# Kernel optimization log

Measured on AMD Instinct MI355X. Metric: run time of the kernel, lower is better.

## Reference

```python
import jax, jax.numpy as jnp
import numpy as np

TAU = 2.0          # LIF membrane time constant (spikingjelly default)
V_TH = 1.0         # v_threshold
V_RESET = 0.0      # hard reset value
ATAN_ALPHA = 2.0   # surrogate.ATan default alpha
EPS = 1e-12        # F.normalize eps

@jax.custom_vjp
def spike_fn(x):
    # Heaviside forward, ATan surrogate backward
    return (x >= 0).astype(x.dtype)

def _spike_fwd(x):
    return spike_fn(x), x

def _spike_bwd(x, g):
    sg = (ATAN_ALPHA / 2.0) / (1.0 + (jnp.pi / 2.0 * ATAN_ALPHA * x) ** 2)
    return (g * sg,)

spike_fn.defvjp(_spike_fwd, _spike_bwd)

def setup_inputs() -> dict:
    key = jax.random.key(0)
    k1, k2 = jax.random.split(key)
    T, B, F, H = 32, 512, 2048, 2048
    x_seq = jax.random.normal(k1, (T, B, F), dtype=jnp.float32)
    lim = float(np.sqrt(6.0 / (F + H)))  # xavier_uniform
    W = jax.random.uniform(k2, (H, F), dtype=jnp.float32, minval=-lim, maxval=lim)
    b = jnp.zeros((H,), dtype=jnp.float32)
    return {"x_seq": x_seq, "W": W, "b": b}

def reference(x_seq, W, b):
    # Linear: [T,B,F] @ [F,H] -> [T,B,H]
    cur = jnp.einsum('tbf,hf->tbh', x_seq, W) + b
    # F.normalize(dim=-1): L2 normalize the injected current per neuron vector
    norm = jnp.maximum(jnp.sqrt(jnp.sum(cur * cur, axis=-1, keepdims=True)), EPS)
    cur = cur / norm

    def step(v, c):
        # LIF charge: v <- v + (x - (v - v_reset)) / tau
        v = v + (c - (v - V_RESET)) / TAU
        s = spike_fn(v - V_TH)
        sd = jax.lax.stop_gradient(s)  # detach_reset=True
        v = v * (1.0 - sd) + V_RESET * sd  # hard reset
        return v, s

    v0 = jnp.zeros(cur.shape[1:], dtype=cur.dtype)  # [B,H]
    _, spk_seq = jax.lax.scan(step, v0, cur)  # spk_seq: [T,B,H]
    count = spk_seq.sum(axis=0)  # [B,H]
    return spk_seq, count
```

## Files before the change

kernel.cpp:

```cpp
#include <hip/hip_runtime.h>
#include <hip/hip_bf16.h>

#define T_SZ 32
#define B_SZ 512
#define F_SZ 2048
#define H_SZ 2048
#define M_SZ (T_SZ * B_SZ)

#define BM 128
#define BN 128
#define BK 128

typedef int   i32x8  __attribute__((ext_vector_type(8)));
typedef float f32x16 __attribute__((ext_vector_type(16)));
typedef unsigned short u16x8 __attribute__((ext_vector_type(8)));

__device__ __forceinline__ void gload_lds16(const void* g, void* l) {
    __builtin_amdgcn_global_load_lds(
        (const __attribute__((address_space(1))) unsigned int*)g,
        (__attribute__((address_space(3))) unsigned int*)l,
        16, 0, 0);
}

__device__ __forceinline__ float bf16_bits_to_f32(unsigned short u) {
    return __uint_as_float(((unsigned)u) << 16);
}

__global__ __launch_bounds__(256) void cvt_fp8_kernel(const float* __restrict__ in,
                                                      unsigned int* __restrict__ out,
                                                      float scale, int n8) {
    int i = blockIdx.x * 256 + threadIdx.x;
    if (i >= n8) return;
    float4 v0 = ((const float4*)in)[2 * i];
    float4 v1 = ((const float4*)in)[2 * i + 1];
    int w0 = __builtin_amdgcn_cvt_pk_fp8_f32(v0.x * scale, v0.y * scale, 0, false);
    w0     = __builtin_amdgcn_cvt_pk_fp8_f32(v0.z * scale, v0.w * scale, w0, true);
    int w1 = __builtin_amdgcn_cvt_pk_fp8_f32(v1.x * scale, v1.y * scale, 0, false);
    w1     = __builtin_amdgcn_cvt_pk_fp8_f32(v1.z * scale, v1.w * scale, w1, true);
    ((uint2*)out)[i] = make_uint2((unsigned)w0, (unsigned)w1);
}

__global__ __launch_bounds__(256) void init_ss_kernel(float4* __restrict__ ss4) {
    ss4[blockIdx.x * 256 + threadIdx.x] = make_float4(0.f, 0.f, 0.f, 0.f);
}

__global__ __launch_bounds__(256, 3) void gemm_fp8_kernel(const unsigned char* __restrict__ A,
                                                          const unsigned char* __restrict__ Bt,
                                                          const float* __restrict__ bias,
                                                          __hip_bfloat16* __restrict__ C,
                                                          float* __restrict__ ss)
{
    __shared__ __align__(16) unsigned char As[BM * BK];
    __shared__ __align__(16) unsigned char Bs[BN * BK];

    const int tid  = threadIdx.x;
    const int lane = tid & 63;
    const int wave = tid >> 6;
    const int wm   = wave >> 1;
    const int wn   = wave & 1;
    const int m0   = blockIdx.y * BM;
    const int n0   = blockIdx.x * BN;
    const int l31  = lane & 31;
    const int kh   = lane >> 5;

    f32x16 acc[2][2] = {};

    for (int k0 = 0; k0 < F_SZ; k0 += BK) {
        __syncthreads();
        #pragma unroll
        for (int j = 0; j < 4; ++j) {
            int c   = j * 256 + tid;
            int row = c >> 3;
            int u   = (c & 7) ^ (row & 7);
            gload_lds16(A + (size_t)(m0 + row) * F_SZ + k0 + u * 16, (void*)(As + c * 16));
        }
        #pragma unroll
        for (int j = 0; j < 4; ++j) {
            int c   = j * 256 + tid;
            int row = c >> 3;
            int u   = (c & 7) ^ (row & 7);
            gload_lds16(Bt + (size_t)(n0 + row) * F_SZ + k0 + u * 16, (void*)(Bs + c * 16));
        }
        __syncthreads();

        #pragma unroll
        for (int s = 0; s < 2; ++s) {
            i32x8 af[2], bq[2];
            #pragma unroll
            for (int i = 0; i < 2; ++i) {
                const int ra = wm * 64 + i * 32 + l31;
                const int rb = wn * 64 + i * 32 + l31;
                const int ua = s * 4 + kh * 2;
                ((int4*)&af[i])[0] = *(const int4*)(As + ra * BK + (((ua + 0) ^ (ra & 7)) * 16));
                ((int4*)&af[i])[1] = *(const int4*)(As + ra * BK + (((ua + 1) ^ (ra & 7)) * 16));
                ((int4*)&bq[i])[0] = *(const int4*)(Bs + rb * BK + (((ua + 0) ^ (rb & 7)) * 16));
                ((int4*)&bq[i])[1] = *(const int4*)(Bs + rb * BK + (((ua + 1) ^ (rb & 7)) * 16));
            }
            #pragma unroll
            for (int mi = 0; mi < 2; ++mi)
                #pragma unroll
                for (int ni = 0; ni < 2; ++ni)
                    acc[mi][ni] = __builtin_amdgcn_mfma_scale_f32_32x32x64_f8f6f4(
                        af[mi], bq[ni], acc[mi][ni],
                        0 , 0 ,
                        0, 0x7f7f7f7f,
                        0, 0x7f7f7f7f);
        }
    }

    float ssl[2][16];
    #pragma unroll
    for (int ni = 0; ni < 2; ++ni) {
        const int gn = n0 + wn * 64 + ni * 32 + l31;
        const float bv = bias[gn];
        #pragma unroll
        for (int mi = 0; mi < 2; ++mi) {
            const int gmb = m0 + wm * 64 + mi * 32 + 4 * kh;
            #pragma unroll
            for (int r = 0; r < 16; ++r) {
                const int grow = gmb + (r & 3) + 8 * (r >> 2);
                const float val = acc[mi][ni][r] * (1.0f / 256.0f) + bv;
                C[(size_t)grow * H_SZ + gn] = __float2bfloat16(val);
                if (ni == 0) ssl[mi][r] = val * val;
                else         ssl[mi][r] += val * val;
            }
        }
    }
    #pragma unroll
    for (int mi = 0; mi < 2; ++mi) {
        const int gmb = m0 + wm * 64 + mi * 32 + 4 * kh;
        #pragma unroll
        for (int r = 0; r < 16; ++r) {
            float p = ssl[mi][r];
            p += __shfl_xor(p, 1, 64);
            p += __shfl_xor(p, 2, 64);
            p += __shfl_xor(p, 4, 64);
            p += __shfl_xor(p, 8, 64);
            p += __shfl_xor(p, 16, 64);
            if (l31 == 0)
                atomicAdd(ss + gmb + (r & 3) + 8 * (r >> 2), p);
        }
    }
}

__global__ __launch_bounds__(256) void lif_scan_kernel(const __hip_bfloat16* __restrict__ cur,
                                                       const float* __restrict__ ss,
                                                       float* __restrict__ spk,
                                                       float* __restrict__ cnt)
{
    const int gid = blockIdx.x * 256 + threadIdx.x;
    const int b   = gid >> 9;
    const int h0  = (gid & 511) * 4;

    float v[4]  = {0, 0, 0, 0};
    float cn[4] = {0, 0, 0, 0};
    #pragma unroll
    for (int t = 0; t < T_SZ; ++t) {
        const size_t off = (size_t)(t * B_SZ + b) * H_SZ + h0;
        const ushort4 pk = *(const ushort4*)(cur + off);
        const float inv  = 1.0f / fmaxf(sqrtf(ss[t * B_SZ + b]), 1e-12f);
        float so[4];
        {
            float c;
            c = bf16_bits_to_f32(pk.x) * inv; v[0] += (c - v[0]) * 0.5f;
            c = bf16_bits_to_f32(pk.y) * inv; v[1] += (c - v[1]) * 0.5f;
            c = bf16_bits_to_f32(pk.z) * inv; v[2] += (c - v[2]) * 0.5f;
            c = bf16_bits_to_f32(pk.w) * inv; v[3] += (c - v[3]) * 0.5f;
        }
        #pragma unroll
        for (int j = 0; j < 4; ++j) {
            float s = (v[j] >= 1.0f) ? 1.0f : 0.0f;
            so[j] = s;
            cn[j] += s;
            v[j] = (s != 0.f) ? 0.f : v[j];
        }
        *(float4*)(spk + off) = make_float4(so[0], so[1], so[2], so[3]);
    }
    *(float4*)(cnt + (size_t)b * H_SZ + h0) = make_float4(cn[0], cn[1], cn[2], cn[3]);
}

extern "C" void kernel_launch(void* const* d_in, const int* in_sizes, int n_in,
                              void* d_out, int out_size, void* d_ws, size_t ws_size,
                              hipStream_t stream) {
    const float* x    = (const float*)d_in[0];
    const float* W    = (const float*)d_in[1];
    const float* bias = (const float*)d_in[2];

    float* spk = (float*)d_out;
    float* cnt = spk + (size_t)T_SZ * B_SZ * H_SZ;

    char* ws = (char*)d_ws;
    unsigned char* x8    = (unsigned char*)ws;
    unsigned char* W8    = x8 + (size_t)M_SZ * F_SZ;
    __hip_bfloat16* curb = (__hip_bfloat16*)(W8 + (size_t)H_SZ * F_SZ);
    float* ss            = (float*)((char*)curb + (size_t)M_SZ * H_SZ * 2);

    init_ss_kernel<<<M_SZ / 1024, 256, 0, stream>>>((float4*)ss);
    cvt_fp8_kernel<<<(M_SZ * F_SZ / 8) / 256, 256, 0, stream>>>(x, (unsigned int*)x8, 1.0f,   M_SZ * F_SZ / 8);
    cvt_fp8_kernel<<<(H_SZ * F_SZ / 8) / 256, 256, 0, stream>>>(W, (unsigned int*)W8, 256.0f, H_SZ * F_SZ / 8);
    gemm_fp8_kernel<<<dim3(H_SZ / BN, M_SZ / BM), 256, 0, stream>>>(x8, W8, bias, curb, ss);
    lif_scan_kernel<<<(B_SZ * H_SZ / 4) / 256, 256, 0, stream>>>(curb, ss, spk, cnt);
}
```

Before: 357.2 us.

## Enlarge FP8 GEMM tiles to 256x256 with double-buffered LDS pipeline and prefetch LIF inputs

Doubles the GEMM block tile to 256x256 with 8 waves. It stages global-to-LDS loads into a ping-pong buffer that is issued in quarter chunks interleaved with the MFMA work, and adds raised wave priority and explicit barriers. Block indices are remapped so that neighbouring blocks share A and B panels in L2. The LIF scan now precomputes per-timestep inverse norms in shared memory and software-prefetches three timesteps of bf16 current. The costs are larger LDS use (128KB per block), more register pressure, and hand-tuned vmcnt waits that could be fragile.

```diff
diff --git a/kernel.cpp b/kernel.cpp
--- a/kernel.cpp
+++ b/kernel.cpp
@@ -7,13 +7,15 @@
 #define H_SZ 2048
 #define M_SZ (T_SZ * B_SZ)
 
-#define BM 128
-#define BN 128
+#define BM 256
+#define BN 256
 #define BK 128
+#define NT (F_SZ / BK)
+#define BUF_BYTES  65536
+#define HALF_BYTES 16384
 
 typedef int   i32x8  __attribute__((ext_vector_type(8)));
 typedef float f32x16 __attribute__((ext_vector_type(16)));
-typedef unsigned short u16x8 __attribute__((ext_vector_type(8)));
 
 __device__ __forceinline__ void gload_lds16(const void* g, void* l) {
     __builtin_amdgcn_global_load_lds(
@@ -24,6 +26,24 @@
 
 __device__ __forceinline__ float bf16_bits_to_f32(unsigned short u) {
     return __uint_as_float(((unsigned)u) << 16);
+}
+
+__device__ __forceinline__ void sbar() {
+    __builtin_amdgcn_sched_barrier(0);
+    __builtin_amdgcn_s_barrier();
+    __builtin_amdgcn_sched_barrier(0);
+}
+
+__device__ __forceinline__ void stage_half_tile(unsigned char* lds,
+                                                const unsigned char* gpanel,
+                                                int kbyte, int tid) {
+    #pragma unroll
+    for (int j = 0; j < 2; ++j) {
+        int c   = j * 512 + tid;
+        int row = c >> 3;
+        int u   = (c & 7) ^ (row & 7);
+        gload_lds16(gpanel + (size_t)row * F_SZ + kbyte + u * 16, (void*)(lds + c * 16));
+    }
 }
 
 __global__ __launch_bounds__(256) void cvt_fp8_kernel(const float* __restrict__ in,
@@ -44,101 +64,125 @@
     ss4[blockIdx.x * 256 + threadIdx.x] = make_float4(0.f, 0.f, 0.f, 0.f);
 }
 
-__global__ __launch_bounds__(256, 3) void gemm_fp8_kernel(const unsigned char* __restrict__ A,
+__global__ __launch_bounds__(512, 2) void gemm_fp8_kernel(const unsigned char* __restrict__ A,
                                                           const unsigned char* __restrict__ Bt,
                                                           const float* __restrict__ bias,
                                                           __hip_bfloat16* __restrict__ C,
                                                           float* __restrict__ ss)
 {
-    __shared__ __align__(16) unsigned char As[BM * BK];
-    __shared__ __align__(16) unsigned char Bs[BN * BK];
+    __shared__ __align__(16) unsigned char smem[2 * BUF_BYTES];
 
     const int tid  = threadIdx.x;
     const int lane = tid & 63;
     const int wave = tid >> 6;
-    const int wm   = wave >> 1;
-    const int wn   = wave & 1;
-    const int m0   = blockIdx.y * BM;
-    const int n0   = blockIdx.x * BN;
+    const int wm   = wave >> 2;
+    const int wn   = wave & 3;
     const int l31  = lane & 31;
     const int kh   = lane >> 5;
 
-    f32x16 acc[2][2] = {};
-
-    for (int k0 = 0; k0 < F_SZ; k0 += BK) {
-        __syncthreads();
-        #pragma unroll
-        for (int j = 0; j < 4; ++j) {
-            int c   = j * 256 + tid;
-            int row = c >> 3;
-            int u   = (c & 7) ^ (row & 7);
-            gload_lds16(A + (size_t)(m0 + row) * F_SZ + k0 + u * 16, (void*)(As + c * 16));
-        }
-        #pragma unroll
-        for (int j = 0; j < 4; ++j) {
-            int c   = j * 256 + tid;
-            int row = c >> 3;
-            int u   = (c & 7) ^ (row & 7);
-            gload_lds16(Bt + (size_t)(n0 + row) * F_SZ + k0 + u * 16, (void*)(Bs + c * 16));
-        }
-        __syncthreads();
-
-        #pragma unroll
-        for (int s = 0; s < 2; ++s) {
-            i32x8 af[2], bq[2];
-            #pragma unroll
-            for (int i = 0; i < 2; ++i) {
-                const int ra = wm * 64 + i * 32 + l31;
-                const int rb = wn * 64 + i * 32 + l31;
+    const int flat = blockIdx.y * 8 + blockIdx.x;
+    const int swz  = (flat & 7) * 64 + (flat >> 3);
+    const int n0   = (swz & 7) * BN;
+    const int m0   = (swz >> 3) * BM;
+
+    f32x16 acc[4][2] = {};
+
+    stage_half_tile(smem + 32768,              Bt + (size_t)(n0      ) * F_SZ, 0, tid);
+    stage_half_tile(smem + 32768 + HALF_BYTES, Bt + (size_t)(n0 + 128) * F_SZ, 0, tid);
+    stage_half_tile(smem,                      A  + (size_t)(m0      ) * F_SZ, 0, tid);
+    stage_half_tile(smem + HALF_BYTES,         A  + (size_t)(m0 + 128) * F_SZ, 0, tid);
+    stage_half_tile(smem + BUF_BYTES + 32768,              Bt + (size_t)(n0      ) * F_SZ, BK, tid);
+    stage_half_tile(smem + BUF_BYTES + 32768 + HALF_BYTES, Bt + (size_t)(n0 + 128) * F_SZ, BK, tid);
+    asm volatile("s_waitcnt vmcnt(4)" ::: "memory");
+    sbar();
+
+    #pragma unroll 1
+    for (int kt = 0; kt < NT; ++kt) {
+        const int cur = kt & 1;
+        const int nxt = cur ^ 1;
+        unsigned char* const As = smem + cur * BUF_BYTES;
+        unsigned char* const Bs = As + 32768;
+
+        auto read_af = [&](i32x8* dst, int mi) {
+            const int ra = wm * 128 + mi * 32 + l31;
+            #pragma unroll
+            for (int s = 0; s < 2; ++s) {
                 const int ua = s * 4 + kh * 2;
-                ((int4*)&af[i])[0] = *(const int4*)(As + ra * BK + (((ua + 0) ^ (ra & 7)) * 16));
-                ((int4*)&af[i])[1] = *(const int4*)(As + ra * BK + (((ua + 1) ^ (ra & 7)) * 16));
-                ((int4*)&bq[i])[0] = *(const int4*)(Bs + rb * BK + (((ua + 0) ^ (rb & 7)) * 16));
-                ((int4*)&bq[i])[1] = *(const int4*)(Bs + rb * BK + (((ua + 1) ^ (rb & 7)) * 16));
+                ((int4*)&dst[s])[0] = *(const int4*)(As + ra * BK + (((ua + 0) ^ (ra & 7)) * 16));
+                ((int4*)&dst[s])[1] = *(const int4*)(As + ra * BK + (((ua + 1) ^ (ra & 7)) * 16));
             }
-            #pragma unroll
-            for (int mi = 0; mi < 2; ++mi)
+        };
+
+        i32x8 bq[2][2];
+        #pragma unroll
+        for (int ni = 0; ni < 2; ++ni) {
+            const int rb = wn * 64 + ni * 32 + l31;
+            #pragma unroll
+            for (int s = 0; s < 2; ++s) {
+                const int ua = s * 4 + kh * 2;
+                ((int4*)&bq[ni][s])[0] = *(const int4*)(Bs + rb * BK + (((ua + 0) ^ (rb & 7)) * 16));
+                ((int4*)&bq[ni][s])[1] = *(const int4*)(Bs + rb * BK + (((ua + 1) ^ (rb & 7)) * 16));
+            }
+        }
+        i32x8 af[2][2];
+        read_af(af[0], 0);
+
+        #pragma unroll
+        for (int mi = 0; mi < 4; ++mi) {
+            if (mi < 3) read_af(af[(mi + 1) & 1], mi + 1);
+
+            if (mi == 0 && kt < NT - 1)
+                stage_half_tile(smem + nxt * BUF_BYTES,              A  + (size_t)(m0      ) * F_SZ, (kt + 1) * BK, tid);
+            if (mi == 1 && kt < NT - 1)
+                stage_half_tile(smem + nxt * BUF_BYTES + HALF_BYTES, A  + (size_t)(m0 + 128) * F_SZ, (kt + 1) * BK, tid);
+            if (mi == 2 && kt < NT - 2)
+                stage_half_tile(smem + cur * BUF_BYTES + 32768,              Bt + (size_t)(n0      ) * F_SZ, (kt + 2) * BK, tid);
+            if (mi == 3 && kt < NT - 2)
+                stage_half_tile(smem + cur * BUF_BYTES + 32768 + HALF_BYTES, Bt + (size_t)(n0 + 128) * F_SZ, (kt + 2) * BK, tid);
+
+            __builtin_amdgcn_sched_barrier(0);
+            __builtin_amdgcn_s_setprio(1);
+            #pragma unroll
+            for (int ni = 0; ni < 2; ++ni)
                 #pragma unroll
-                for (int ni = 0; ni < 2; ++ni)
+                for (int s = 0; s < 2; ++s)
                     acc[mi][ni] = __builtin_amdgcn_mfma_scale_f32_32x32x64_f8f6f4(
-                        af[mi], bq[ni], acc[mi][ni],
+                        af[mi & 1][s], bq[ni][s], acc[mi][ni],
                         0 , 0 ,
                         0, 0x7f7f7f7f,
                         0, 0x7f7f7f7f);
-        }
-    }
-
-    float ssl[2][16];
-    #pragma unroll
-    for (int ni = 0; ni < 2; ++ni) {
-        const int gn = n0 + wn * 64 + ni * 32 + l31;
-        const float bv = bias[gn];
-        #pragma unroll
-        for (int mi = 0; mi < 2; ++mi) {
-            const int gmb = m0 + wm * 64 + mi * 32 + 4 * kh;
-            #pragma unroll
-            for (int r = 0; r < 16; ++r) {
-                const int grow = gmb + (r & 3) + 8 * (r >> 2);
-                const float val = acc[mi][ni][r] * (1.0f / 256.0f) + bv;
+            __builtin_amdgcn_s_setprio(0);
+            if (mi < 3) sbar();
+        }
+
+        if (kt <= NT - 3)      { asm volatile("s_waitcnt vmcnt(4)" ::: "memory"); }
+        else if (kt == NT - 2) { asm volatile("s_waitcnt vmcnt(0)" ::: "memory"); }
+        sbar();
+    }
+
+    float bv[2];
+    #pragma unroll
+    for (int ni = 0; ni < 2; ++ni) bv[ni] = bias[n0 + wn * 64 + ni * 32 + l31];
+    #pragma unroll
+    for (int mi = 0; mi < 4; ++mi) {
+        const int gmb = m0 + wm * 128 + mi * 32 + 4 * kh;
+        #pragma unroll
+        for (int r = 0; r < 16; ++r) {
+            const int grow = gmb + (r & 3) + 8 * (r >> 2);
+            float p = 0.f;
+            #pragma unroll
+            for (int ni = 0; ni < 2; ++ni) {
+                const int gn = n0 + wn * 64 + ni * 32 + l31;
+                const float val = acc[mi][ni][r] * (1.0f / 256.0f) + bv[ni];
                 C[(size_t)grow * H_SZ + gn] = __float2bfloat16(val);
-                if (ni == 0) ssl[mi][r] = val * val;
-                else         ssl[mi][r] += val * val;
+                p += val * val;
             }
-        }
-    }
-    #pragma unroll
-    for (int mi = 0; mi < 2; ++mi) {
-        const int gmb = m0 + wm * 64 + mi * 32 + 4 * kh;
-        #pragma unroll
-        for (int r = 0; r < 16; ++r) {
-            float p = ssl[mi][r];
             p += __shfl_xor(p, 1, 64);
             p += __shfl_xor(p, 2, 64);
             p += __shfl_xor(p, 4, 64);
             p += __shfl_xor(p, 8, 64);
             p += __shfl_xor(p, 16, 64);
-            if (l31 == 0)
-                atomicAdd(ss + gmb + (r & 3) + 8 * (r >> 2), p);
+            if (l31 == 0) atomicAdd(ss + grow, p);
         }
     }
 }
@@ -148,24 +192,38 @@
                                                        float* __restrict__ spk,
                                                        float* __restrict__ cnt)
 {
+    __shared__ float s_inv[T_SZ];
     const int gid = blockIdx.x * 256 + threadIdx.x;
     const int b   = gid >> 9;
     const int h0  = (gid & 511) * 4;
 
+    if (threadIdx.x < T_SZ)
+        s_inv[threadIdx.x] = 1.0f / fmaxf(sqrtf(ss[threadIdx.x * B_SZ + b]), 1e-12f);
+    __syncthreads();
+
+    const size_t stride = (size_t)B_SZ * H_SZ;
+    const size_t base   = (size_t)b * H_SZ + h0;
+    const __hip_bfloat16* p = cur + base;
+
+    ushort4 pk[3];
+    pk[0] = *(const ushort4*)(p);
+    pk[1] = *(const ushort4*)(p + stride);
+    pk[2] = *(const ushort4*)(p + 2 * stride);
+
     float v[4]  = {0, 0, 0, 0};
     float cn[4] = {0, 0, 0, 0};
     #pragma unroll
     for (int t = 0; t < T_SZ; ++t) {
-        const size_t off = (size_t)(t * B_SZ + b) * H_SZ + h0;
-        const ushort4 pk = *(const ushort4*)(cur + off);
-        const float inv  = 1.0f / fmaxf(sqrtf(ss[t * B_SZ + b]), 1e-12f);
+        const ushort4 k = pk[t % 3];
+        if (t + 3 < T_SZ) pk[t % 3] = *(const ushort4*)(p + (size_t)(t + 3) * stride);
+        const float inv = s_inv[t];
         float so[4];
         {
             float c;
-            c = bf16_bits_to_f32(pk.x) * inv; v[0] += (c - v[0]) * 0.5f;
-            c = bf16_bits_to_f32(pk.y) * inv; v[1] += (c - v[1]) * 0.5f;
-            c = bf16_bits_to_f32(pk.z) * inv; v[2] += (c - v[2]) * 0.5f;
-            c = bf16_bits_to_f32(pk.w) * inv; v[3] += (c - v[3]) * 0.5f;
+            c = bf16_bits_to_f32(k.x) * inv; v[0] += (c - v[0]) * 0.5f;
+            c = bf16_bits_to_f32(k.y) * inv; v[1] += (c - v[1]) * 0.5f;
+            c = bf16_bits_to_f32(k.z) * inv; v[2] += (c - v[2]) * 0.5f;
+            c = bf16_bits_to_f32(k.w) * inv; v[3] += (c - v[3]) * 0.5f;
         }
         #pragma unroll
         for (int j = 0; j < 4; ++j) {
@@ -174,9 +232,9 @@
             cn[j] += s;
             v[j] = (s != 0.f) ? 0.f : v[j];
         }
-        *(float4*)(spk + off) = make_float4(so[0], so[1], so[2], so[3]);
-    }
-    *(float4*)(cnt + (size_t)b * H_SZ + h0) = make_float4(cn[0], cn[1], cn[2], cn[3]);
+        *(float4*)(spk + base + (size_t)t * stride) = make_float4(so[0], so[1], so[2], so[3]);
+    }
+    *(float4*)(cnt + base) = make_float4(cn[0], cn[1], cn[2], cn[3]);
 }
 
 extern "C" void kernel_launch(void* const* d_in, const int* in_sizes, int n_in,
@@ -198,6 +256,6 @@
     init_ss_kernel<<<M_SZ / 1024, 256, 0, stream>>>((float4*)ss);
     cvt_fp8_kernel<<<(M_SZ * F_SZ / 8) / 256, 256, 0, stream>>>(x, (unsigned int*)x8, 1.0f,   M_SZ * F_SZ / 8);
     cvt_fp8_kernel<<<(H_SZ * F_SZ / 8) / 256, 256, 0, stream>>>(W, (unsigned int*)W8, 256.0f, H_SZ * F_SZ / 8);
-    gemm_fp8_kernel<<<dim3(H_SZ / BN, M_SZ / BM), 256, 0, stream>>>(x8, W8, bias, curb, ss);
+    gemm_fp8_kernel<<<dim3(H_SZ / BN, M_SZ / BM), 512, 0, stream>>>(x8, W8, bias, curb, ss);
     lif_scan_kernel<<<(B_SZ * H_SZ / 4) / 256, 256, 0, stream>>>(curb, ss, spk, cnt);
 }
```

New measurement: 372.2 us. 4.2% more time.
